# Kernel optimization log

Measured on AMD Instinct MI355X. Metric: run time of the kernel, lower is better.

The kernel has to match this reference:

```python
import jax, jax.numpy as jnp
import numpy as np
from jax import lax

LRELU_SLOPE = 0.2
GAIN = 2.0 ** 0.5
EPS = 1e-8


def setup_inputs() -> dict:
    key = jax.random.key(0)
    ks = jax.random.split(key, 8)
    B, NDW, CIN, COUT, H, W = 4, 512, 16, 16, 1024, 1024
    return {
        "w": jax.random.normal(ks[0], (B, NDW), jnp.float32),
        "x": jax.random.normal(ks[1], (B, CIN, H, W), jnp.float32),
        "noise": jax.random.normal(ks[2], (B, 1, H, W), jnp.float32),
        "fc_weight": jax.random.normal(ks[3], (CIN, NDW), jnp.float32),
        "fc_bias": jnp.ones((CIN,), jnp.float32),
        "conv_weight": jax.random.normal(ks[4], (COUT, CIN, 3, 3), jnp.float32),
        "conv_bias": jax.random.normal(ks[5], (COUT,), jnp.float32),
        "scale_noise": jnp.float32(0.1),
    }


def reference(w, x, noise, fc_weight, fc_bias, conv_weight, conv_bias, scale_noise):
    NDW = fc_weight.shape[1]
    COUT, CIN, KH, KW = conv_weight.shape
    # equal_lr scaling (FC): weight * n_dim_in**-0.5
    s = w @ (fc_weight.T * (NDW ** -0.5)) + fc_bias  # [B, CIN] style per input channel
    # equal_lr scaling (Conv): weight * (in_channels * k^2)**-0.5
    wc = conv_weight * ((CIN * KH * KW) ** -0.5)  # [COUT, CIN, 3, 3]
    # demodulation coefficient: d[b,o] = 1/sqrt(sum_{i,kh,kw} (s[b,i]*wc[o,i,kh,kw])^2 + eps)
    w2 = (wc ** 2).sum(axis=(2, 3))  # [COUT, CIN]
    d = lax.rsqrt((s ** 2) @ w2.T + EPS)  # [B, COUT]
    # modulate input instead of materializing per-sample weights (mathematically identical)
    xm = x * s[:, :, None, None]
    y = lax.conv_general_dilated(
        xm, wc, window_strides=(1, 1), padding=((1, 1), (1, 1)),
        dimension_numbers=("NCHW", "OIHW", "NCHW"))
    y = y * d[:, :, None, None] + conv_bias[None, :, None, None]
    y = y + scale_noise * noise  # broadcast noise over channels
    y = GAIN * jnp.where(y >= 0, y, LRELU_SLOPE * y)
    return (w, y)
```

## Files before the change

kernel.cpp:

```cpp
#include <hip/hip_runtime.h>

#define H_ 1024
#define W_ 1024
#define B_ 4
#define CIN 16
#define COUT 16
#define TH 8
#define TW 64
#define NT 8
#define ROWS 10
#define COLS 66

#define LRELU 0.2f
#define GAIN_ 1.4142135623730951f
#define EPS_ 1e-8f

#define BAR_LGKM()                                                      \
    do {                                                                \
        __builtin_amdgcn_sched_barrier(0);                              \
        asm volatile("s_waitcnt lgkmcnt(0)\n\ts_barrier" ::: "memory"); \
        __builtin_amdgcn_sched_barrier(0);                              \
    } while (0)

typedef __attribute__((ext_vector_type(8))) short bf16x8;
typedef __attribute__((ext_vector_type(4))) float f32x4;

static __device__ __forceinline__ unsigned short f32_to_bf16(float f) {
    unsigned int u = __float_as_uint(f);
    unsigned int r = u + 0x7FFF + ((u >> 16) & 1);
    return (unsigned short)(r >> 16);
}

static __device__ __forceinline__ float f4c(const float4& v, int px) {
    return px == 0 ? v.x : px == 1 ? v.y : px == 2 ? v.z : v.w;
}

__global__ __launch_bounds__(256) void k_setup1(
    const float* __restrict__ w, const float* __restrict__ fcw,
    const float* __restrict__ fcb, float* __restrict__ s_out,
    float* __restrict__ w_copy_out)
{
    __shared__ float part[256];
    const int tid = threadIdx.x;
    const int bi = tid >> 2;
    const int q  = tid & 3;
    const int b = bi >> 4, i = bi & 15;
    const float* wr = w + b * 512 + q * 128;
    const float* fr = fcw + i * 512 + q * 128;
    float acc = 0.f;
    #pragma unroll 8
    for (int k = 0; k < 128; ++k) acc += wr[k] * fr[k];
    part[tid] = acc;
    __syncthreads();
    if (tid < 64) {
        float v = part[tid*4] + part[tid*4+1] + part[tid*4+2] + part[tid*4+3];
        s_out[tid] = v * 0.04419417382415922f  + fcb[tid & 15];
    }
    for (int e = tid; e < B_ * 512; e += 256) w_copy_out[e] = w[e];
}

__global__ __launch_bounds__(256) void k_setup2(
    const float* __restrict__ s_in, const float* __restrict__ convw,
    unsigned short* __restrict__ afrag)
{
    const int b = blockIdx.x;
    const int tid = threadIdx.x;
    __shared__ float s_sh[16];
    __shared__ float d_sh[16];
    __shared__ float wc_sh[COUT * CIN * 9];
    __shared__ float part[256];

    if (tid < 16) s_sh[tid] = s_in[b * 16 + tid];
    for (int e = tid; e < COUT * CIN * 9; e += 256)
        wc_sh[e] = convw[e] * (1.0f / 12.0f);
    __syncthreads();

    const int o = tid >> 4, i = tid & 15;
    const float si = s_sh[i];
    float acc = 0.f;
    #pragma unroll
    for (int tap = 0; tap < 9; ++tap) {
        float v = wc_sh[(o * 16 + i) * 9 + tap] * si;
        acc += v * v;
    }
    part[tid] = acc;
    __syncthreads();
    if (tid < 16) {
        float sum = EPS_;
        #pragma unroll
        for (int j = 0; j < 16; ++j) sum += part[tid * 16 + j];
        d_sh[tid] = rsqrtf(sum);
    }
    __syncthreads();

    for (int e = tid; e < 5 * 64 * 8; e += 256) {
        int t = e >> 9;
        int lane = (e >> 3) & 63;
        int j = e & 7;
        int oo = lane & 15, g = lane >> 4;
        int ii = (g & 1) * 8 + j;
        int tap = 2 * t + (g >> 1);
        float v = 0.f;
        if (tap < 9) v = wc_sh[(oo * 16 + ii) * 9 + tap] * s_sh[ii] * d_sh[oo];
        afrag[(size_t)b * (5 * 64 * 8) + e] = f32_to_bf16(v);
    }
}

__global__ __launch_bounds__(256) void k_conv(
    const float* __restrict__ x, const float* __restrict__ noise,
    const float* __restrict__ conv_bias, const float* __restrict__ sn_ptr,
    const unsigned short* __restrict__ afrag, float* __restrict__ y)
{
    __shared__ unsigned short tile[2][ROWS][COLS][8];

    const int tid = threadIdx.x;
    const int bt = blockIdx.z;
    const int h0s = blockIdx.y * (TH * NT);
    const int w0 = blockIdx.x * TW;
    const float sn = sn_ptr[0];
    const float* xb = x + (size_t)bt * CIN * H_ * W_;
    float* yb = y + (size_t)bt * COUT * H_ * W_;
    const float* nb = noise + (size_t)bt * H_ * W_;

    const int lane  = tid & 63;
    const int wid   = tid >> 6;
    const int p     = lane & 15;
    const int g     = lane >> 4;
    const int ghalf = g >> 1;
    const int chalf = g & 1;

    const int rowA = tid >> 5, subA = tid & 31, hhA = subA >> 4, cgA = subA & 15;
    const int rowB = 8 + (tid >> 5);
    const bool hasB = (tid < 64);
    const bool hasE = (tid >= 64) && (tid < 104);
    const int e_  = tid - 64;
    const int rowE = e_ >> 2, sideE = (e_ >> 1) & 1, hhE = e_ & 1;

    float4 vA[8], vB[8];
    float  ev[8];

    auto stage_load = [&](int t) {
        const int gh0 = h0s + TH * t - 1;
        {
            const int gh = gh0 + rowA;
            const bool ok = (gh >= 0) && (gh < H_);
            const float* base = xb + ((size_t)(8 * hhA) * H_ + gh) * W_ + (w0 + 4 * cgA);
            #pragma unroll
            for (int c = 0; c < 8; ++c) {
                vA[c] = make_float4(0.f, 0.f, 0.f, 0.f);
                if (ok) vA[c] = *reinterpret_cast<const float4*>(base + (size_t)c * H_ * W_);
            }
        }
        if (hasB) {
            const int gh = gh0 + rowB;
            const bool ok = (gh >= 0) && (gh < H_);
            const float* base = xb + ((size_t)(8 * hhA) * H_ + gh) * W_ + (w0 + 4 * cgA);
            #pragma unroll
            for (int c = 0; c < 8; ++c) {
                vB[c] = make_float4(0.f, 0.f, 0.f, 0.f);
                if (ok) vB[c] = *reinterpret_cast<const float4*>(base + (size_t)c * H_ * W_);
            }
        } else if (hasE) {
            const int gh = gh0 + rowE;
            const int gw = w0 - 1 + sideE * (COLS - 1);
            const bool ok = (gh >= 0) && (gh < H_) && (gw >= 0) && (gw < W_);
            #pragma unroll
            for (int c = 0; c < 8; ++c)
                ev[c] = ok ? xb[((size_t)(8 * hhE + c) * H_ + gh) * W_ + gw] : 0.f;
        }
    };

    auto stage_write = [&]() {
        #pragma unroll
        for (int px = 0; px < 4; ++px) {
            bf16x8 pk;
            #pragma unroll
            for (int c = 0; c < 8; ++c) pk[c] = (short)f32_to_bf16(f4c(vA[c], px));
            *reinterpret_cast<bf16x8*>(&tile[hhA][rowA][1 + 4 * cgA + px][0]) = pk;
        }
        if (hasB) {
            #pragma unroll
            for (int px = 0; px < 4; ++px) {
                bf16x8 pk;
                #pragma unroll
                for (int c = 0; c < 8; ++c) pk[c] = (short)f32_to_bf16(f4c(vB[c], px));
                *reinterpret_cast<bf16x8*>(&tile[hhA][rowB][1 + 4 * cgA + px][0]) = pk;
            }
        } else if (hasE) {
            bf16x8 pk;
            #pragma unroll
            for (int c = 0; c < 8; ++c) pk[c] = (short)f32_to_bf16(ev[c]);
            *reinterpret_cast<bf16x8*>(&tile[hhE][rowE][sideE * (COLS - 1)][0]) = pk;
        }
    };

    bf16x8 a[5];
    {
        const bf16x8* ap = reinterpret_cast<const bf16x8*>(afrag + (size_t)bt * 5 * 64 * 8);
        #pragma unroll
        for (int t = 0; t < 5; ++t) a[t] = ap[t * 64 + lane];
    }
    float bias_j[4];
    #pragma unroll
    for (int j = 0; j < 4; ++j) bias_j[j] = conv_bias[g * 4 + j];

    int lroff[5], lcoff[5];
    #pragma unroll
    for (int t = 0; t < 5; ++t) {
        int tap = 2 * t + ghalf;
        if (tap > 8) tap = 8;
        lroff[t] = tap / 3;
        lcoff[t] = tap % 3;
    }

    auto compute = [&](int t) {
        #pragma unroll
        for (int rr = 0; rr < 2; ++rr) {
            const int oh = wid * 2 + rr;
            const int gh = h0s + TH * t + oh;
            #pragma unroll
            for (int gc = 0; gc < 4; ++gc) {
                const int ow = gc * 16;
                f32x4 acc = {0.f, 0.f, 0.f, 0.f};
                #pragma unroll
                for (int tt = 0; tt < 5; ++tt) {
                    const bf16x8 bv = *reinterpret_cast<const bf16x8*>(
                        &tile[chalf][oh + lroff[tt]][ow + p + lcoff[tt]][0]);
                    acc = __builtin_amdgcn_mfma_f32_16x16x32_bf16(a[tt], bv, acc, 0, 0, 0);
                }
                const int gw = w0 + ow + p;
                const float noi = nb[(size_t)gh * W_ + gw] * sn;
                #pragma unroll
                for (int j = 0; j < 4; ++j) {
                    float vv = acc[j] + bias_j[j] + noi;
                    vv = (vv >= 0.f) ? vv : (LRELU * vv);
                    yb[((size_t)(g * 4 + j) * H_ + gh) * W_ + gw] = vv * GAIN_;
                }
            }
        }
    };

    stage_load(0);
    for (int t = 0; t < NT; ++t) {
        if (t > 0) BAR_LGKM();
        stage_write();
        BAR_LGKM();
        if (t + 1 < NT) stage_load(t + 1);
        compute(t);
    }
}

extern "C" void kernel_launch(void* const* d_in, const int* in_sizes, int n_in,
                              void* d_out, int out_size, void* d_ws, size_t ws_size,
                              hipStream_t stream)
{
    const float* w     = (const float*)d_in[0];
    const float* x     = (const float*)d_in[1];
    const float* noise = (const float*)d_in[2];
    const float* fcw   = (const float*)d_in[3];
    const float* fcb   = (const float*)d_in[4];
    const float* convw = (const float*)d_in[5];
    const float* convb = (const float*)d_in[6];
    const float* sn    = (const float*)d_in[7];

    float* out = (float*)d_out;
    float* ws_s = (float*)d_ws;
    unsigned short* ws_afrag = (unsigned short*)((char*)d_ws + 256);

    k_setup1<<<1, 256, 0, stream>>>(w, fcw, fcb, ws_s, out);
    k_setup2<<<B_, 256, 0, stream>>>(ws_s, convw, ws_afrag);
    dim3 grid(W_ / TW, H_ / (TH * NT), B_);
    k_conv<<<grid, 256, 0, stream>>>(x, noise, convb, sn, ws_afrag, out + 2048);
}
```

Before: 172.7 us.

## Switch conv to 32x32x16 MFMA with row-split tap packing and swizzled LDS

Repacks the modulated and demodulated weights into six fragments, P and Q, for the 32x32x16 bf16 MFMA. Each wave computes 4 output rows by 32 columns for all 16 channels, and the partial sums of adjacent rows are combined to cover the 3x3 taps. The LDS tile gets a column swizzle to avoid bank conflicts. A fifth wave is added that only stages the halo rows and edge columns, and each block now processes 16 row stages instead of 8. The aim is fewer LDS fragment reads and better overlap of staging with compute, at the cost of some zero-padded MFMA work and a grid with half as many blocks.

```diff
diff --git a/kernel.cpp b/kernel.cpp
--- a/kernel.cpp
+++ b/kernel.cpp
@@ -7,9 +7,9 @@
 #define COUT 16
 #define TH 8
 #define TW 64
-#define NT 8
+#define NT 16
 #define ROWS 10
-#define COLS 66
+#define COLS_U 74
 
 #define LRELU 0.2f
 #define GAIN_ 1.4142135623730951f
@@ -23,7 +23,7 @@
     } while (0)
 
 typedef __attribute__((ext_vector_type(8))) short bf16x8;
-typedef __attribute__((ext_vector_type(4))) float f32x4;
+typedef __attribute__((ext_vector_type(16))) float f32x16;
 
 static __device__ __forceinline__ unsigned short f32_to_bf16(float f) {
     unsigned int u = __float_as_uint(f);
@@ -34,6 +34,8 @@
 static __device__ __forceinline__ float f4c(const float4& v, int px) {
     return px == 0 ? v.x : px == 1 ? v.y : px == 2 ? v.z : v.w;
 }
+
+static __device__ __forceinline__ int swz(int c) { return c + (c >> 3); }
 
 __global__ __launch_bounds__(256) void k_setup1(
     const float* __restrict__ w, const float* __restrict__ fcw,
@@ -93,25 +95,30 @@
     }
     __syncthreads();
 
-    for (int e = tid; e < 5 * 64 * 8; e += 256) {
-        int t = e >> 9;
-        int lane = (e >> 3) & 63;
-        int j = e & 7;
-        int oo = lane & 15, g = lane >> 4;
-        int ii = (g & 1) * 8 + j;
-        int tap = 2 * t + (g >> 1);
+    for (int e = tid; e < 6 * 64 * 8; e += 256) {
+        const int f    = e >> 9;
+        const int lane = (e >> 3) & 63;
+        const int j    = e & 7;
+        const int C    = (f < 3) ? f : (f - 3);
+        const bool isQ = (f >= 3);
+        const int oo = lane & 15;
+        const int R  = (lane >> 4) & 1;
+        const int ii = 8 * (lane >> 5) + j;
+        int tap;
+        if (!isQ) tap = 3 * R + C;
+        else      tap = (R == 0) ? (6 + C) : -1;
         float v = 0.f;
-        if (tap < 9) v = wc_sh[(oo * 16 + ii) * 9 + tap] * s_sh[ii] * d_sh[oo];
-        afrag[(size_t)b * (5 * 64 * 8) + e] = f32_to_bf16(v);
-    }
-}
-
-__global__ __launch_bounds__(256) void k_conv(
+        if (tap >= 0) v = wc_sh[(oo * 16 + ii) * 9 + tap] * s_sh[ii] * d_sh[oo];
+        afrag[(size_t)b * (6 * 64 * 8) + e] = f32_to_bf16(v);
+    }
+}
+
+__global__ __launch_bounds__(320) void k_conv(
     const float* __restrict__ x, const float* __restrict__ noise,
     const float* __restrict__ conv_bias, const float* __restrict__ sn_ptr,
     const unsigned short* __restrict__ afrag, float* __restrict__ y)
 {
-    __shared__ unsigned short tile[2][ROWS][COLS][8];
+    __shared__ unsigned short tile[2][ROWS][COLS_U][8];
 
     const int tid = threadIdx.x;
     const int bt = blockIdx.z;
@@ -122,47 +129,35 @@
     float* yb = y + (size_t)bt * COUT * H_ * W_;
     const float* nb = noise + (size_t)bt * H_ * W_;
 
-    const int lane  = tid & 63;
-    const int wid   = tid >> 6;
-    const int p     = lane & 15;
-    const int g     = lane >> 4;
-    const int ghalf = g >> 1;
-    const int chalf = g & 1;
-
-    const int rowA = tid >> 5, subA = tid & 31, hhA = subA >> 4, cgA = subA & 15;
-    const int rowB = 8 + (tid >> 5);
-    const bool hasB = (tid < 64);
-    const bool hasE = (tid >= 64) && (tid < 104);
-    const int e_  = tid - 64;
+    const int lane = tid & 63;
+    const int wid  = tid >> 6;
+
+    const int rowS = tid >> 5;
+    const int subS = tid & 31;
+    const int hhS  = subS >> 4;
+    const int cgS  = subS & 15;
+    const bool hasE = (tid >= 256) && (tid < 296);
+    const int e_   = tid - 256;
     const int rowE = e_ >> 2, sideE = (e_ >> 1) & 1, hhE = e_ & 1;
 
-    float4 vA[8], vB[8];
+    float4 vS[8];
     float  ev[8];
 
     auto stage_load = [&](int t) {
         const int gh0 = h0s + TH * t - 1;
         {
-            const int gh = gh0 + rowA;
+            const int gh = gh0 + rowS;
             const bool ok = (gh >= 0) && (gh < H_);
-            const float* base = xb + ((size_t)(8 * hhA) * H_ + gh) * W_ + (w0 + 4 * cgA);
+            const float* base = xb + ((size_t)(8 * hhS) * H_ + gh) * W_ + (w0 + 4 * cgS);
             #pragma unroll
             for (int c = 0; c < 8; ++c) {
-                vA[c] = make_float4(0.f, 0.f, 0.f, 0.f);
-                if (ok) vA[c] = *reinterpret_cast<const float4*>(base + (size_t)c * H_ * W_);
-            }
-        }
-        if (hasB) {
-            const int gh = gh0 + rowB;
-            const bool ok = (gh >= 0) && (gh < H_);
-            const float* base = xb + ((size_t)(8 * hhA) * H_ + gh) * W_ + (w0 + 4 * cgA);
-            #pragma unroll
-            for (int c = 0; c < 8; ++c) {
-                vB[c] = make_float4(0.f, 0.f, 0.f, 0.f);
-                if (ok) vB[c] = *reinterpret_cast<const float4*>(base + (size_t)c * H_ * W_);
-            }
-        } else if (hasE) {
+                vS[c] = make_float4(0.f, 0.f, 0.f, 0.f);
+                if (ok) vS[c] = *reinterpret_cast<const float4*>(base + (size_t)c * H_ * W_);
+            }
+        }
+        if (hasE) {
             const int gh = gh0 + rowE;
-            const int gw = w0 - 1 + sideE * (COLS - 1);
+            const int gw = w0 - 1 + sideE * 65;
             const bool ok = (gh >= 0) && (gh < H_) && (gw >= 0) && (gw < W_);
             #pragma unroll
             for (int c = 0; c < 8; ++c)
@@ -175,66 +170,81 @@
         for (int px = 0; px < 4; ++px) {
             bf16x8 pk;
             #pragma unroll
-            for (int c = 0; c < 8; ++c) pk[c] = (short)f32_to_bf16(f4c(vA[c], px));
-            *reinterpret_cast<bf16x8*>(&tile[hhA][rowA][1 + 4 * cgA + px][0]) = pk;
-        }
-        if (hasB) {
-            #pragma unroll
-            for (int px = 0; px < 4; ++px) {
-                bf16x8 pk;
+            for (int c = 0; c < 8; ++c) pk[c] = (short)f32_to_bf16(f4c(vS[c], px));
+            const int u = swz(1 + 4 * cgS + px);
+            *reinterpret_cast<bf16x8*>(&tile[hhS][rowS][u][0]) = pk;
+        }
+        if (hasE) {
+            bf16x8 pk;
+            #pragma unroll
+            for (int c = 0; c < 8; ++c) pk[c] = (short)f32_to_bf16(ev[c]);
+            const int u = sideE ? swz(65) : 0;
+            *reinterpret_cast<bf16x8*>(&tile[hhE][rowE][u][0]) = pk;
+        }
+    };
+
+    const int s_ = wid & 1;
+    const int g_ = (wid >> 1) & 1;
+    const int baseRow = 4 * s_;
+    const int colBase = g_ * 32 + (lane & 31);
+    const int chalfB  = lane >> 5;
+
+    bf16x8 aP[3], aQ[3];
+    {
+        const bf16x8* ap = reinterpret_cast<const bf16x8*>(afrag + (size_t)bt * 6 * 64 * 8);
+        #pragma unroll
+        for (int C = 0; C < 3; ++C) {
+            aP[C] = ap[C * 64 + lane];
+            aQ[C] = ap[(3 + C) * 64 + lane];
+        }
+    }
+    int   o_j[8];
+    float bias_j[8];
+    #pragma unroll
+    for (int j = 0; j < 8; ++j) {
+        o_j[j] = (j & 3) + 8 * (j >> 2) + 4 * chalfB;
+        bias_j[j] = conv_bias[o_j[j]];
+    }
+
+    auto compute = [&](int t) {
+        if (wid >= 4) return;
+        const int ghBase = h0s + TH * t + 4 * s_;
+        f32x16 zro;
+        #pragma unroll
+        for (int i = 0; i < 16; ++i) zro[i] = 0.f;
+        f32x16 cacc[5];
+        #pragma unroll
+        for (int k = 0; k < 6; ++k) {
+            bf16x8 bv0, bv1, bv2;
+            {
+                const unsigned short* rbase = &tile[chalfB][baseRow + k][0][0];
+                const int c0 = colBase,     u0 = swz(c0);
+                const int c1 = colBase + 1, u1 = swz(c1);
+                const int c2 = colBase + 2, u2 = swz(c2);
+                bv0 = *reinterpret_cast<const bf16x8*>(&rbase[u0 * 8]);
+                bv1 = *reinterpret_cast<const bf16x8*>(&rbase[u1 * 8]);
+                bv2 = *reinterpret_cast<const bf16x8*>(&rbase[u2 * 8]);
+            }
+            if (k <= 4) {
+                f32x16 t0 = __builtin_amdgcn_mfma_f32_32x32x16_bf16(aP[0], bv0, zro, 0, 0, 0);
+                t0 = __builtin_amdgcn_mfma_f32_32x32x16_bf16(aP[1], bv1, t0, 0, 0, 0);
+                t0 = __builtin_amdgcn_mfma_f32_32x32x16_bf16(aP[2], bv2, t0, 0, 0, 0);
+                cacc[k] = t0;
+            }
+            if (k >= 2) {
+                f32x16 t1 = cacc[k - 2];
+                t1 = __builtin_amdgcn_mfma_f32_32x32x16_bf16(aQ[0], bv0, t1, 0, 0, 0);
+                t1 = __builtin_amdgcn_mfma_f32_32x32x16_bf16(aQ[1], bv1, t1, 0, 0, 0);
+                t1 = __builtin_amdgcn_mfma_f32_32x32x16_bf16(aQ[2], bv2, t1, 0, 0, 0);
+                cacc[k - 2] = t1;
+                const int r = k - 2;
+                const int gh = ghBase + r;
+                const float noi = nb[(size_t)gh * W_ + w0 + colBase] * sn;
                 #pragma unroll
-                for (int c = 0; c < 8; ++c) pk[c] = (short)f32_to_bf16(f4c(vB[c], px));
-                *reinterpret_cast<bf16x8*>(&tile[hhA][rowB][1 + 4 * cgA + px][0]) = pk;
-            }
-        } else if (hasE) {
-            bf16x8 pk;
-            #pragma unroll
-            for (int c = 0; c < 8; ++c) pk[c] = (short)f32_to_bf16(ev[c]);
-            *reinterpret_cast<bf16x8*>(&tile[hhE][rowE][sideE * (COLS - 1)][0]) = pk;
-        }
-    };
-
-    bf16x8 a[5];
-    {
-        const bf16x8* ap = reinterpret_cast<const bf16x8*>(afrag + (size_t)bt * 5 * 64 * 8);
-        #pragma unroll
-        for (int t = 0; t < 5; ++t) a[t] = ap[t * 64 + lane];
-    }
-    float bias_j[4];
-    #pragma unroll
-    for (int j = 0; j < 4; ++j) bias_j[j] = conv_bias[g * 4 + j];
-
-    int lroff[5], lcoff[5];
-    #pragma unroll
-    for (int t = 0; t < 5; ++t) {
-        int tap = 2 * t + ghalf;
-        if (tap > 8) tap = 8;
-        lroff[t] = tap / 3;
-        lcoff[t] = tap % 3;
-    }
-
-    auto compute = [&](int t) {
-        #pragma unroll
-        for (int rr = 0; rr < 2; ++rr) {
-            const int oh = wid * 2 + rr;
-            const int gh = h0s + TH * t + oh;
-            #pragma unroll
-            for (int gc = 0; gc < 4; ++gc) {
-                const int ow = gc * 16;
-                f32x4 acc = {0.f, 0.f, 0.f, 0.f};
-                #pragma unroll
-                for (int tt = 0; tt < 5; ++tt) {
-                    const bf16x8 bv = *reinterpret_cast<const bf16x8*>(
-                        &tile[chalf][oh + lroff[tt]][ow + p + lcoff[tt]][0]);
-                    acc = __builtin_amdgcn_mfma_f32_16x16x32_bf16(a[tt], bv, acc, 0, 0, 0);
-                }
-                const int gw = w0 + ow + p;
-                const float noi = nb[(size_t)gh * W_ + gw] * sn;
-                #pragma unroll
-                for (int j = 0; j < 4; ++j) {
-                    float vv = acc[j] + bias_j[j] + noi;
-                    vv = (vv >= 0.f) ? vv : (LRELU * vv);
-                    yb[((size_t)(g * 4 + j) * H_ + gh) * W_ + gw] = vv * GAIN_;
+                for (int j = 0; j < 8; ++j) {
+                    float v = cacc[k - 2][j] + cacc[k - 1][8 + j] + bias_j[j] + noi;
+                    v = (v >= 0.f) ? v : (LRELU * v);
+                    yb[((size_t)o_j[j] * H_ + gh) * W_ + w0 + colBase] = v * GAIN_;
                 }
             }
         }
@@ -270,5 +280,5 @@
     k_setup1<<<1, 256, 0, stream>>>(w, fcw, fcb, ws_s, out);
     k_setup2<<<B_, 256, 0, stream>>>(ws_s, convw, ws_afrag);
     dim3 grid(W_ / TW, H_ / (TH * NT), B_);
-    k_conv<<<grid, 256, 0, stream>>>(x, noise, convb, sn, ws_afrag, out + 2048);
-}
+    k_conv<<<grid, 320, 0, stream>>>(x, noise, convb, sn, ws_afrag, out + 2048);
+}
```

After: 167.6 us. 3.0% less time.

## Shrink conv row tile, redistribute staging loads, swizzle LDS, prefetch noise

Applied to the files above, without the earlier changes.

The output row tile per stage is halved and the global-to-LDS staging is redistributed so every thread loads 2-channel float4 pairs across three slots. This drops the large per-thread staging register arrays, and a launch-bounds hint of 6 blocks per CU is added to raise occupancy. LDS columns get a padding swizzle to reduce bank conflicts. Noise values are prefetched before the barrier, and MFMA sections are bracketed with raised wave priority. In exchange, the vertical halo becomes a larger share of each tile, so more redundant input rows are read per output row.

```diff
diff --git a/kernel.cpp b/kernel.cpp
--- a/kernel.cpp
+++ b/kernel.cpp
@@ -5,11 +5,11 @@
 #define B_ 4
 #define CIN 16
 #define COUT 16
-#define TH 8
+#define TH 4
 #define TW 64
 #define NT 8
-#define ROWS 10
-#define COLS 66
+#define ROWS 6
+#define COLS_U 74
 
 #define LRELU 0.2f
 #define GAIN_ 1.4142135623730951f
@@ -34,6 +34,8 @@
 static __device__ __forceinline__ float f4c(const float4& v, int px) {
     return px == 0 ? v.x : px == 1 ? v.y : px == 2 ? v.z : v.w;
 }
+
+static __device__ __forceinline__ int swz(int c) { return c + (c >> 3); }
 
 __global__ __launch_bounds__(256) void k_setup1(
     const float* __restrict__ w, const float* __restrict__ fcw,
@@ -106,12 +108,12 @@
     }
 }
 
-__global__ __launch_bounds__(256) void k_conv(
+__global__ __launch_bounds__(256, 6) void k_conv(
     const float* __restrict__ x, const float* __restrict__ noise,
     const float* __restrict__ conv_bias, const float* __restrict__ sn_ptr,
     const unsigned short* __restrict__ afrag, float* __restrict__ y)
 {
-    __shared__ unsigned short tile[2][ROWS][COLS][8];
+    __shared__ unsigned short tile[2][ROWS][COLS_U][8];
 
     const int tid = threadIdx.x;
     const int bt = blockIdx.z;
@@ -129,40 +131,38 @@
     const int ghalf = g >> 1;
     const int chalf = g & 1;
 
-    const int rowA = tid >> 5, subA = tid & 31, hhA = subA >> 4, cgA = subA & 15;
-    const int rowB = 8 + (tid >> 5);
-    const bool hasB = (tid < 64);
-    const bool hasE = (tid >= 64) && (tid < 104);
-    const int e_  = tid - 64;
-    const int rowE = e_ >> 2, sideE = (e_ >> 1) & 1, hhE = e_ & 1;
-
-    float4 vA[8], vB[8];
+    int s_row[3], s_ch2[3], s_cg[3];
+    #pragma unroll
+    for (int k = 0; k < 3; ++k) {
+        const int u = k * 256 + tid;
+        s_row[k] = u >> 7;
+        s_ch2[k] = (u >> 4) & 7;
+        s_cg[k]  = u & 15;
+    }
+    const bool hasE = (tid < 24);
+    const int rowE = tid >> 2, sideE = (tid >> 1) & 1, hhE = tid & 1;
+
+    float4 vS[3][2];
     float  ev[8];
+    float  nv[4];
 
     auto stage_load = [&](int t) {
         const int gh0 = h0s + TH * t - 1;
-        {
-            const int gh = gh0 + rowA;
+        #pragma unroll
+        for (int k = 0; k < 3; ++k) {
+            const int gh = gh0 + s_row[k];
             const bool ok = (gh >= 0) && (gh < H_);
-            const float* base = xb + ((size_t)(8 * hhA) * H_ + gh) * W_ + (w0 + 4 * cgA);
-            #pragma unroll
-            for (int c = 0; c < 8; ++c) {
-                vA[c] = make_float4(0.f, 0.f, 0.f, 0.f);
-                if (ok) vA[c] = *reinterpret_cast<const float4*>(base + (size_t)c * H_ * W_);
-            }
-        }
-        if (hasB) {
-            const int gh = gh0 + rowB;
-            const bool ok = (gh >= 0) && (gh < H_);
-            const float* base = xb + ((size_t)(8 * hhA) * H_ + gh) * W_ + (w0 + 4 * cgA);
-            #pragma unroll
-            for (int c = 0; c < 8; ++c) {
-                vB[c] = make_float4(0.f, 0.f, 0.f, 0.f);
-                if (ok) vB[c] = *reinterpret_cast<const float4*>(base + (size_t)c * H_ * W_);
-            }
-        } else if (hasE) {
+            const float* base =
+                xb + ((size_t)(2 * s_ch2[k]) * H_ + gh) * W_ + (w0 + 4 * s_cg[k]);
+            #pragma unroll
+            for (int c = 0; c < 2; ++c) {
+                vS[k][c] = make_float4(0.f, 0.f, 0.f, 0.f);
+                if (ok) vS[k][c] = *reinterpret_cast<const float4*>(base + (size_t)c * H_ * W_);
+            }
+        }
+        if (hasE) {
             const int gh = gh0 + rowE;
-            const int gw = w0 - 1 + sideE * (COLS - 1);
+            const int gw = w0 - 1 + sideE * 65;
             const bool ok = (gh >= 0) && (gh < H_) && (gw >= 0) && (gw < W_);
             #pragma unroll
             for (int c = 0; c < 8; ++c)
@@ -172,25 +172,22 @@
 
     auto stage_write = [&]() {
         #pragma unroll
-        for (int px = 0; px < 4; ++px) {
+        for (int k = 0; k < 3; ++k) {
+            const int hh  = s_ch2[k] >> 2;
+            const int chq = (s_ch2[k] & 3) * 2;
+            #pragma unroll
+            for (int px = 0; px < 4; ++px) {
+                const unsigned int lo = f32_to_bf16(f4c(vS[k][0], px));
+                const unsigned int hi = f32_to_bf16(f4c(vS[k][1], px));
+                unsigned short* dst = &tile[hh][s_row[k]][swz(1 + 4 * s_cg[k] + px)][chq];
+                *reinterpret_cast<unsigned int*>(dst) = lo | (hi << 16);
+            }
+        }
+        if (hasE) {
             bf16x8 pk;
             #pragma unroll
-            for (int c = 0; c < 8; ++c) pk[c] = (short)f32_to_bf16(f4c(vA[c], px));
-            *reinterpret_cast<bf16x8*>(&tile[hhA][rowA][1 + 4 * cgA + px][0]) = pk;
-        }
-        if (hasB) {
-            #pragma unroll
-            for (int px = 0; px < 4; ++px) {
-                bf16x8 pk;
-                #pragma unroll
-                for (int c = 0; c < 8; ++c) pk[c] = (short)f32_to_bf16(f4c(vB[c], px));
-                *reinterpret_cast<bf16x8*>(&tile[hhA][rowB][1 + 4 * cgA + px][0]) = pk;
-            }
-        } else if (hasE) {
-            bf16x8 pk;
-            #pragma unroll
             for (int c = 0; c < 8; ++c) pk[c] = (short)f32_to_bf16(ev[c]);
-            *reinterpret_cast<bf16x8*>(&tile[hhE][rowE][sideE * (COLS - 1)][0]) = pk;
+            *reinterpret_cast<bf16x8*>(&tile[hhE][rowE][sideE ? swz(65) : 0][0]) = pk;
         }
     };
 
@@ -213,36 +210,43 @@
         lcoff[t] = tap % 3;
     }
 
+    auto noise_prefetch = [&](int t) {
+        const int gh = h0s + TH * t + wid;
+        #pragma unroll
+        for (int gc = 0; gc < 4; ++gc)
+            nv[gc] = nb[(size_t)gh * W_ + w0 + gc * 16 + p];
+    };
+
     auto compute = [&](int t) {
-        #pragma unroll
-        for (int rr = 0; rr < 2; ++rr) {
-            const int oh = wid * 2 + rr;
-            const int gh = h0s + TH * t + oh;
-            #pragma unroll
-            for (int gc = 0; gc < 4; ++gc) {
-                const int ow = gc * 16;
-                f32x4 acc = {0.f, 0.f, 0.f, 0.f};
-                #pragma unroll
-                for (int tt = 0; tt < 5; ++tt) {
-                    const bf16x8 bv = *reinterpret_cast<const bf16x8*>(
-                        &tile[chalf][oh + lroff[tt]][ow + p + lcoff[tt]][0]);
-                    acc = __builtin_amdgcn_mfma_f32_16x16x32_bf16(a[tt], bv, acc, 0, 0, 0);
-                }
-                const int gw = w0 + ow + p;
-                const float noi = nb[(size_t)gh * W_ + gw] * sn;
-                #pragma unroll
-                for (int j = 0; j < 4; ++j) {
-                    float vv = acc[j] + bias_j[j] + noi;
-                    vv = (vv >= 0.f) ? vv : (LRELU * vv);
-                    yb[((size_t)(g * 4 + j) * H_ + gh) * W_ + gw] = vv * GAIN_;
-                }
-            }
-        }
+        const int oh = wid;
+        const int gh = h0s + TH * t + oh;
+        __builtin_amdgcn_s_setprio(1);
+        #pragma unroll
+        for (int gc = 0; gc < 4; ++gc) {
+            const int ow = gc * 16;
+            f32x4 acc = {0.f, 0.f, 0.f, 0.f};
+            #pragma unroll
+            for (int tt = 0; tt < 5; ++tt) {
+                const bf16x8 bv = *reinterpret_cast<const bf16x8*>(
+                    &tile[chalf][oh + lroff[tt]][swz(ow + p + lcoff[tt])][0]);
+                acc = __builtin_amdgcn_mfma_f32_16x16x32_bf16(a[tt], bv, acc, 0, 0, 0);
+            }
+            const int gw = w0 + ow + p;
+            const float noi = nv[gc] * sn;
+            #pragma unroll
+            for (int j = 0; j < 4; ++j) {
+                float vv = acc[j] + bias_j[j] + noi;
+                vv = (vv >= 0.f) ? vv : (LRELU * vv);
+                yb[((size_t)(g * 4 + j) * H_ + gh) * W_ + gw] = vv * GAIN_;
+            }
+        }
+        __builtin_amdgcn_s_setprio(0);
     };
 
     stage_load(0);
     for (int t = 0; t < NT; ++t) {
         if (t > 0) BAR_LGKM();
+        noise_prefetch(t);
         stage_write();
         BAR_LGKM();
         if (t + 1 < NT) stage_load(t + 1);
```

After: 511.9 us. +196.4%, slower.
